# Performance work log

Hardware: AMD Instinct MI355X
Metric: run time of the kernel (lower is better)

## Reference

```python
import jax, jax.numpy as jnp
import numpy as np

USER_SIZE = 100000
ITEM_SIZE = 100000
EMBED = 64
BATCH = 16384


def _xavier(key, fan_in, fan_out):
    # xavier_uniform for a torch Linear(fan_in, fan_out); stored as [in, out]
    limit = float(np.sqrt(6.0 / (fan_in + fan_out)))
    return jax.random.uniform(key, (fan_in, fan_out), jnp.float32, -limit, limit)


def setup_inputs() -> dict:
    key = jax.random.key(0)
    ks = jax.random.split(key, 12)
    inp = {
        "user": jax.random.randint(ks[0], (BATCH,), 0, USER_SIZE),
        "item": jax.random.randint(ks[1], (BATCH,), 0, ITEM_SIZE),
        # embedding tables = Linear(vocab, embed) weights, stored [vocab, embed]
        "W_user_gmf": _xavier(ks[2], USER_SIZE, EMBED),
        "b_user_gmf": jnp.zeros((EMBED,), jnp.float32),
        "W_user_mlp": _xavier(ks[3], USER_SIZE, EMBED),
        "b_user_mlp": jnp.zeros((EMBED,), jnp.float32),
        "W_item_gmf": _xavier(ks[4], ITEM_SIZE, EMBED),
        "b_item_gmf": jnp.zeros((EMBED,), jnp.float32),
        "W_item_mlp": _xavier(ks[5], ITEM_SIZE, EMBED),
        "b_item_mlp": jnp.zeros((EMBED,), jnp.float32),
        # MLP tower (eval mode -> dropout is identity)
        "W1": _xavier(ks[6], 2 * EMBED, 2 * EMBED),
        "b1": jnp.zeros((2 * EMBED,), jnp.float32),
        "W2": _xavier(ks[7], 2 * EMBED, EMBED),
        "b2": jnp.zeros((EMBED,), jnp.float32),
        "W3": _xavier(ks[8], EMBED, EMBED // 2),
        "b3": jnp.zeros((EMBED // 2,), jnp.float32),
        "Wp": _xavier(ks[9], EMBED * 3 // 2, 1),
        "bp": jnp.zeros((1,), jnp.float32),
    }
    return inp


def reference(user, item, W_user_gmf, b_user_gmf, W_user_mlp, b_user_mlp,
              W_item_gmf, b_item_gmf, W_item_mlp, b_item_mlp,
              W1, b1, W2, b2, W3, b3, Wp, bp):
    # one-hot @ Linear(vocab, embed) == row gather from the weight table + bias
    eu_gmf = jax.nn.relu(W_user_gmf[user] + b_user_gmf)  # [B, E]
    eu_mlp = jax.nn.relu(W_user_mlp[user] + b_user_mlp)
    ei_gmf = jax.nn.relu(W_item_gmf[item] + b_item_gmf)
    ei_mlp = jax.nn.relu(W_item_mlp[item] + b_item_mlp)

    out_gmf = eu_gmf * ei_gmf                             # [B, E]
    h = jnp.concatenate([eu_mlp, ei_mlp], axis=-1)        # [B, 2E]
    h = jax.nn.relu(h @ W1 + b1)                          # [B, 2E]
    h = jax.nn.relu(h @ W2 + b2)                          # [B, E]
    h = jax.nn.relu(h @ W3 + b3)                          # [B, E/2]

    concat = jnp.concatenate([out_gmf, h], axis=-1)       # [B, 3E/2]
    pred = jax.nn.sigmoid(concat @ Wp + bp)               # [B, 1]
    return pred.reshape(-1)
```

## Files before the change

kernel.cpp:

```cpp
#include <hip/hip_runtime.h>
#include <math.h>

typedef __attribute__((ext_vector_type(8))) short bf16x8;
typedef __attribute__((ext_vector_type(4))) float f32x4;

#define TPB  256
#define NBLK 256

#define W1T_OFF 0
#define W2T_OFF 34816
#define W3T_OFF 52224
#define SCR_OFF 56832
#define SCR_PW  4352
#define SM_BYTES (SCR_OFF + 4*SCR_PW)

__device__ __forceinline__ unsigned short f2bf(float a){
  unsigned ua = __float_as_uint(a);
  return (unsigned short)((ua + 0x7FFFu + ((ua>>16)&1u)) >> 16);
}
__device__ __forceinline__ unsigned int f2bf_pk(float a, float b){
  return (unsigned int)f2bf(a) | ((unsigned int)f2bf(b) << 16);
}
__device__ __forceinline__ bf16x8 mk_frag(float4 a, float4 ba, float4 b, float4 bb){
  union { bf16x8 v; unsigned int u[4]; } o;
  o.u[0] = f2bf_pk(fmaxf(a.x+ba.x,0.f), fmaxf(a.y+ba.y,0.f));
  o.u[1] = f2bf_pk(fmaxf(a.z+ba.z,0.f), fmaxf(a.w+ba.w,0.f));
  o.u[2] = f2bf_pk(fmaxf(b.x+bb.x,0.f), fmaxf(b.y+bb.y,0.f));
  o.u[3] = f2bf_pk(fmaxf(b.z+bb.z,0.f), fmaxf(b.w+bb.w,0.f));
  return o.v;
}

__launch_bounds__(TPB, 2)
__global__ void ncf_mfma(
    const int* __restrict__ user, const int* __restrict__ item,
    const float* __restrict__ Wug, const float* __restrict__ bug,
    const float* __restrict__ Wum, const float* __restrict__ bum,
    const float* __restrict__ Wig, const float* __restrict__ big,
    const float* __restrict__ Wim, const float* __restrict__ bim,
    const float* __restrict__ W1, const float* __restrict__ b1,
    const float* __restrict__ W2, const float* __restrict__ b2,
    const float* __restrict__ W3, const float* __restrict__ b3,
    const float* __restrict__ Wp, const float* __restrict__ bp,
    float* __restrict__ out)
{
  extern __shared__ __align__(16) char sm[];
  const int t    = threadIdx.x;
  const int lane = t & 63;
  const int w    = t >> 6;
  const int r    = lane & 15;
  const int g    = lane >> 4;
  const int gb   = blockIdx.x * 64 + w * 16 + r;

  const int u  = user[gb];
  const int it = item[gb];
  const float* up = Wum + (size_t)u  * 64;
  const float* ip = Wim + (size_t)it * 64;
  float4 mu0 = *(const float4*)(up + 8*g);
  float4 mu1 = *(const float4*)(up + 8*g + 4);
  float4 mu2 = *(const float4*)(up + 32 + 8*g);
  float4 mu3 = *(const float4*)(up + 32 + 8*g + 4);
  float4 mi0 = *(const float4*)(ip + 8*g);
  float4 mi1 = *(const float4*)(ip + 8*g + 4);
  float4 mi2 = *(const float4*)(ip + 32 + 8*g);
  float4 mi3 = *(const float4*)(ip + 32 + 8*g + 4);
  float4 bu0 = *(const float4*)(bum + 8*g);
  float4 bu1 = *(const float4*)(bum + 8*g + 4);
  float4 bu2 = *(const float4*)(bum + 32 + 8*g);
  float4 bu3 = *(const float4*)(bum + 32 + 8*g + 4);
  float4 bi0 = *(const float4*)(bim + 8*g);
  float4 bi1 = *(const float4*)(bim + 8*g + 4);
  float4 bi2 = *(const float4*)(bim + 32 + 8*g);
  float4 bi3 = *(const float4*)(bim + 32 + 8*g + 4);

  const float* ugp = Wug + (size_t)u  * 64 + 16*g;
  const float* igp = Wig + (size_t)it * 64 + 16*g;
  float4 ga[4], gi[4], gba[4], gbb[4], wpv[4];
  #pragma unroll
  for (int c = 0; c < 4; ++c) {
    ga[c]  = *(const float4*)(ugp + 4*c);
    gi[c]  = *(const float4*)(igp + 4*c);
    gba[c] = *(const float4*)(bug + 16*g + 4*c);
    gbb[c] = *(const float4*)(big + 16*g + 4*c);
    wpv[c] = *(const float4*)(Wp  + 16*g + 4*c);
  }
  float b1v[8], b2v[4], b3v[2], wp3[2];
  #pragma unroll
  for (int i = 0; i < 8; ++i) b1v[i] = b1[i*16 + r];
  #pragma unroll
  for (int i = 0; i < 4; ++i) b2v[i] = b2[i*16 + r];
  #pragma unroll
  for (int i = 0; i < 2; ++i) { b3v[i] = b3[i*16 + r]; wp3[i] = Wp[64 + i*16 + r]; }
  const float bpv = bp[0];

  #pragma unroll
  for (int i = 0; i < 32; ++i) {
    int p = i*TPB + t; int n = p & 127, kp = p >> 7;
    float f0 = W1[(2*kp)*128 + n], f1 = W1[(2*kp+1)*128 + n];
    *(unsigned int*)(sm + W1T_OFF + n*272 + kp*4) = f2bf_pk(f0, f1);
  }
  #pragma unroll
  for (int i = 0; i < 16; ++i) {
    int p = i*TPB + t; int n = p & 63, kp = p >> 6;
    float f0 = W2[(2*kp)*64 + n], f1 = W2[(2*kp+1)*64 + n];
    *(unsigned int*)(sm + W2T_OFF + n*272 + kp*4) = f2bf_pk(f0, f1);
  }
  #pragma unroll
  for (int i = 0; i < 4; ++i) {
    int p = i*TPB + t; int n = p & 31, kp = p >> 5;
    float f0 = W3[(2*kp)*32 + n], f1 = W3[(2*kp+1)*32 + n];
    *(unsigned int*)(sm + W3T_OFF + n*144 + kp*4) = f2bf_pk(f0, f1);
  }

  float psum = 0.f;
  #pragma unroll
  for (int c = 0; c < 4; ++c) {
    psum += fmaxf(ga[c].x+gba[c].x,0.f) * fmaxf(gi[c].x+gbb[c].x,0.f) * wpv[c].x;
    psum += fmaxf(ga[c].y+gba[c].y,0.f) * fmaxf(gi[c].y+gbb[c].y,0.f) * wpv[c].y;
    psum += fmaxf(ga[c].z+gba[c].z,0.f) * fmaxf(gi[c].z+gbb[c].z,0.f) * wpv[c].z;
    psum += fmaxf(ga[c].w+gba[c].w,0.f) * fmaxf(gi[c].w+gbb[c].w,0.f) * wpv[c].w;
  }

  bf16x8 afr[4];
  afr[0] = mk_frag(mu0, bu0, mu1, bu1);
  afr[1] = mk_frag(mu2, bu2, mu3, bu3);
  afr[2] = mk_frag(mi0, bi0, mi1, bi1);
  afr[3] = mk_frag(mi2, bi2, mi3, bi3);

  __syncthreads();

  char* scr = sm + SCR_OFF + w * SCR_PW;

  #pragma unroll
  for (int nt = 0; nt < 8; ++nt) {
    f32x4 acc = {b1v[nt], b1v[nt], b1v[nt], b1v[nt]};
    #pragma unroll
    for (int s = 0; s < 4; ++s) {
      bf16x8 bf = *(const bf16x8*)(sm + W1T_OFF + (nt*16 + r)*272 + s*64 + g*16);
      acc = __builtin_amdgcn_mfma_f32_16x16x32_bf16(afr[s], bf, acc, 0, 0, 0);
    }
    #pragma unroll
    for (int q = 0; q < 4; ++q)
      *(unsigned short*)(scr + (4*g + q)*272 + (nt*16 + r)*2) = f2bf(fmaxf(acc[q], 0.f));
  }

  bf16x8 a2[4];
  #pragma unroll
  for (int s = 0; s < 4; ++s)
    a2[s] = *(const bf16x8*)(scr + r*272 + s*64 + g*16);
  #pragma unroll
  for (int nt = 0; nt < 4; ++nt) {
    f32x4 acc = {b2v[nt], b2v[nt], b2v[nt], b2v[nt]};
    #pragma unroll
    for (int s = 0; s < 4; ++s) {
      bf16x8 bf = *(const bf16x8*)(sm + W2T_OFF + (nt*16 + r)*272 + s*64 + g*16);
      acc = __builtin_amdgcn_mfma_f32_16x16x32_bf16(a2[s], bf, acc, 0, 0, 0);
    }
    #pragma unroll
    for (int q = 0; q < 4; ++q)
      *(unsigned short*)(scr + (4*g + q)*144 + (nt*16 + r)*2) = f2bf(fmaxf(acc[q], 0.f));
  }

  bf16x8 a3[2];
  #pragma unroll
  for (int s = 0; s < 2; ++s)
    a3[s] = *(const bf16x8*)(scr + r*144 + s*64 + g*16);
  float h3p[4] = {0.f, 0.f, 0.f, 0.f};
  #pragma unroll
  for (int nt = 0; nt < 2; ++nt) {
    f32x4 acc = {b3v[nt], b3v[nt], b3v[nt], b3v[nt]};
    #pragma unroll
    for (int s = 0; s < 2; ++s) {
      bf16x8 bf = *(const bf16x8*)(sm + W3T_OFF + (nt*16 + r)*144 + s*64 + g*16);
      acc = __builtin_amdgcn_mfma_f32_16x16x32_bf16(a3[s], bf, acc, 0, 0, 0);
    }
    #pragma unroll
    for (int q = 0; q < 4; ++q)
      h3p[q] += fmaxf(acc[q], 0.f) * wp3[nt];
  }

  float* scf = (float*)scr;
  #pragma unroll
  for (int q = 0; q < 4; ++q) scf[(4*g + q)*20 + r] = h3p[q];
  scf[r*20 + 16 + g] = psum;
  __builtin_amdgcn_wave_barrier();

  if (lane < 16) {
    float x = bpv;
    const float4* row = (const float4*)(scf + lane*20);
    #pragma unroll
    for (int i = 0; i < 5; ++i) { float4 v = row[i]; x += v.x + v.y + v.z + v.w; }
    out[blockIdx.x*64 + w*16 + lane] = 1.f / (1.f + expf(-x));
  }
}

extern "C" void kernel_launch(void* const* d_in, const int* in_sizes, int n_in,
                              void* d_out, int out_size, void* d_ws, size_t ws_size,
                              hipStream_t stream) {
  const int*   user = (const int*)  d_in[0];
  const int*   item = (const int*)  d_in[1];
  const float* Wug  = (const float*)d_in[2];
  const float* bug  = (const float*)d_in[3];
  const float* Wum  = (const float*)d_in[4];
  const float* bum  = (const float*)d_in[5];
  const float* Wig  = (const float*)d_in[6];
  const float* big  = (const float*)d_in[7];
  const float* Wim  = (const float*)d_in[8];
  const float* bim  = (const float*)d_in[9];
  const float* W1   = (const float*)d_in[10];
  const float* b1   = (const float*)d_in[11];
  const float* W2   = (const float*)d_in[12];
  const float* b2   = (const float*)d_in[13];
  const float* W3   = (const float*)d_in[14];
  const float* b3   = (const float*)d_in[15];
  const float* Wp   = (const float*)d_in[16];
  const float* bp   = (const float*)d_in[17];
  float* out = (float*)d_out;

  (void)hipFuncSetAttribute(reinterpret_cast<const void*>(ncf_mfma),
                            hipFuncAttributeMaxDynamicSharedMemorySize, SM_BYTES);
  ncf_mfma<<<NBLK, TPB, SM_BYTES, stream>>>(
      user, item, Wug, bug, Wum, bum, Wig, big, Wim, bim,
      W1, b1, W2, b2, W3, b3, Wp, bp, out);
}
```

Measured before the change: 12.63 us.

## Split GMF and MLP work across separate waves in 512-thread blocks

```diff
diff --git a/kernel.cpp b/kernel.cpp
--- a/kernel.cpp
+++ b/kernel.cpp
@@ -4,7 +4,7 @@
 typedef __attribute__((ext_vector_type(8))) short bf16x8;
 typedef __attribute__((ext_vector_type(4))) float f32x4;
 
-#define TPB  256
+#define TPB  512
 #define NBLK 256
 
 #define W1T_OFF 0
@@ -12,7 +12,8 @@
 #define W3T_OFF 52224
 #define SCR_OFF 56832
 #define SCR_PW  4352
-#define SM_BYTES (SCR_OFF + 4*SCR_PW)
+#define PG_OFF  74240
+#define SM_BYTES (PG_OFF + 1024)
 
 __device__ __forceinline__ unsigned short f2bf(float a){
   unsigned ua = __float_as_uint(a);
@@ -49,147 +50,156 @@
   const int w    = t >> 6;
   const int r    = lane & 15;
   const int g    = lane >> 4;
-  const int gb   = blockIdx.x * 64 + w * 16 + r;
-
-  const int u  = user[gb];
-  const int it = item[gb];
-  const float* up = Wum + (size_t)u  * 64;
-  const float* ip = Wim + (size_t)it * 64;
-  float4 mu0 = *(const float4*)(up + 8*g);
-  float4 mu1 = *(const float4*)(up + 8*g + 4);
-  float4 mu2 = *(const float4*)(up + 32 + 8*g);
-  float4 mu3 = *(const float4*)(up + 32 + 8*g + 4);
-  float4 mi0 = *(const float4*)(ip + 8*g);
-  float4 mi1 = *(const float4*)(ip + 8*g + 4);
-  float4 mi2 = *(const float4*)(ip + 32 + 8*g);
-  float4 mi3 = *(const float4*)(ip + 32 + 8*g + 4);
-  float4 bu0 = *(const float4*)(bum + 8*g);
-  float4 bu1 = *(const float4*)(bum + 8*g + 4);
-  float4 bu2 = *(const float4*)(bum + 32 + 8*g);
-  float4 bu3 = *(const float4*)(bum + 32 + 8*g + 4);
-  float4 bi0 = *(const float4*)(bim + 8*g);
-  float4 bi1 = *(const float4*)(bim + 8*g + 4);
-  float4 bi2 = *(const float4*)(bim + 32 + 8*g);
-  float4 bi3 = *(const float4*)(bim + 32 + 8*g + 4);
-
-  const float* ugp = Wug + (size_t)u  * 64 + 16*g;
-  const float* igp = Wig + (size_t)it * 64 + 16*g;
+  const bool twv = (w < 4);
+  const int  tw  = twv ? w : (w - 4);
+  const int  gb  = blockIdx.x * 64 + tw * 16 + r;
+
+  float4 mu0, mu1, mu2, mu3, mi0, mi1, mi2, mi3;
+  float4 bu0, bu1, bu2, bu3, bi0, bi1, bi2, bi3;
+  float  b1v[8], b2v[4], b3v[2], wp3[2], bpv = 0.f;
   float4 ga[4], gi[4], gba[4], gbb[4], wpv[4];
+
+  if (twv) {
+    const int u  = user[gb];
+    const int it = item[gb];
+    const float* up = Wum + (size_t)u  * 64;
+    const float* ip = Wim + (size_t)it * 64;
+    mu0 = *(const float4*)(up + 8*g);       mu1 = *(const float4*)(up + 8*g + 4);
+    mu2 = *(const float4*)(up + 32 + 8*g);  mu3 = *(const float4*)(up + 32 + 8*g + 4);
+    mi0 = *(const float4*)(ip + 8*g);       mi1 = *(const float4*)(ip + 8*g + 4);
+    mi2 = *(const float4*)(ip + 32 + 8*g);  mi3 = *(const float4*)(ip + 32 + 8*g + 4);
+    bu0 = *(const float4*)(bum + 8*g);      bu1 = *(const float4*)(bum + 8*g + 4);
+    bu2 = *(const float4*)(bum + 32 + 8*g); bu3 = *(const float4*)(bum + 32 + 8*g + 4);
+    bi0 = *(const float4*)(bim + 8*g);      bi1 = *(const float4*)(bim + 8*g + 4);
+    bi2 = *(const float4*)(bim + 32 + 8*g); bi3 = *(const float4*)(bim + 32 + 8*g + 4);
+    #pragma unroll
+    for (int i = 0; i < 8; ++i) b1v[i] = b1[i*16 + r];
+    #pragma unroll
+    for (int i = 0; i < 4; ++i) b2v[i] = b2[i*16 + r];
+    #pragma unroll
+    for (int i = 0; i < 2; ++i) { b3v[i] = b3[i*16 + r]; wp3[i] = Wp[64 + i*16 + r]; }
+    bpv = bp[0];
+  } else {
+    const int u  = user[gb];
+    const int it = item[gb];
+    const float* ugp = Wug + (size_t)u  * 64 + 16*g;
+    const float* igp = Wig + (size_t)it * 64 + 16*g;
+    #pragma unroll
+    for (int c = 0; c < 4; ++c) {
+      ga[c]  = *(const float4*)(ugp + 4*c);
+      gi[c]  = *(const float4*)(igp + 4*c);
+      gba[c] = *(const float4*)(bug + 16*g + 4*c);
+      gbb[c] = *(const float4*)(big + 16*g + 4*c);
+      wpv[c] = *(const float4*)(Wp  + 16*g + 4*c);
+    }
+  }
+
   #pragma unroll
-  for (int c = 0; c < 4; ++c) {
-    ga[c]  = *(const float4*)(ugp + 4*c);
-    gi[c]  = *(const float4*)(igp + 4*c);
-    gba[c] = *(const float4*)(bug + 16*g + 4*c);
-    gbb[c] = *(const float4*)(big + 16*g + 4*c);
-    wpv[c] = *(const float4*)(Wp  + 16*g + 4*c);
-  }
-  float b1v[8], b2v[4], b3v[2], wp3[2];
-  #pragma unroll
-  for (int i = 0; i < 8; ++i) b1v[i] = b1[i*16 + r];
-  #pragma unroll
-  for (int i = 0; i < 4; ++i) b2v[i] = b2[i*16 + r];
-  #pragma unroll
-  for (int i = 0; i < 2; ++i) { b3v[i] = b3[i*16 + r]; wp3[i] = Wp[64 + i*16 + r]; }
-  const float bpv = bp[0];
-
-  #pragma unroll
-  for (int i = 0; i < 32; ++i) {
+  for (int i = 0; i < 16; ++i) {
     int p = i*TPB + t; int n = p & 127, kp = p >> 7;
     float f0 = W1[(2*kp)*128 + n], f1 = W1[(2*kp+1)*128 + n];
     *(unsigned int*)(sm + W1T_OFF + n*272 + kp*4) = f2bf_pk(f0, f1);
   }
   #pragma unroll
-  for (int i = 0; i < 16; ++i) {
+  for (int i = 0; i < 8; ++i) {
     int p = i*TPB + t; int n = p & 63, kp = p >> 6;
     float f0 = W2[(2*kp)*64 + n], f1 = W2[(2*kp+1)*64 + n];
     *(unsigned int*)(sm + W2T_OFF + n*272 + kp*4) = f2bf_pk(f0, f1);
   }
   #pragma unroll
-  for (int i = 0; i < 4; ++i) {
+  for (int i = 0; i < 2; ++i) {
     int p = i*TPB + t; int n = p & 31, kp = p >> 5;
     float f0 = W3[(2*kp)*32 + n], f1 = W3[(2*kp+1)*32 + n];
     *(unsigned int*)(sm + W3T_OFF + n*144 + kp*4) = f2bf_pk(f0, f1);
   }
 
-  float psum = 0.f;
-  #pragma unroll
-  for (int c = 0; c < 4; ++c) {
-    psum += fmaxf(ga[c].x+gba[c].x,0.f) * fmaxf(gi[c].x+gbb[c].x,0.f) * wpv[c].x;
-    psum += fmaxf(ga[c].y+gba[c].y,0.f) * fmaxf(gi[c].y+gbb[c].y,0.f) * wpv[c].y;
-    psum += fmaxf(ga[c].z+gba[c].z,0.f) * fmaxf(gi[c].z+gbb[c].z,0.f) * wpv[c].z;
-    psum += fmaxf(ga[c].w+gba[c].w,0.f) * fmaxf(gi[c].w+gbb[c].w,0.f) * wpv[c].w;
-  }
-
   bf16x8 afr[4];
-  afr[0] = mk_frag(mu0, bu0, mu1, bu1);
-  afr[1] = mk_frag(mu2, bu2, mu3, bu3);
-  afr[2] = mk_frag(mi0, bi0, mi1, bi1);
-  afr[3] = mk_frag(mi2, bi2, mi3, bi3);
+  if (twv) {
+    afr[0] = mk_frag(mu0, bu0, mu1, bu1);
+    afr[1] = mk_frag(mu2, bu2, mu3, bu3);
+    afr[2] = mk_frag(mi0, bi0, mi1, bi1);
+    afr[3] = mk_frag(mi2, bi2, mi3, bi3);
+  } else {
+    float psum = 0.f;
+    #pragma unroll
+    for (int c = 0; c < 4; ++c) {
+      psum += fmaxf(ga[c].x+gba[c].x,0.f) * fmaxf(gi[c].x+gbb[c].x,0.f) * wpv[c].x;
+      psum += fmaxf(ga[c].y+gba[c].y,0.f) * fmaxf(gi[c].y+gbb[c].y,0.f) * wpv[c].y;
+      psum += fmaxf(ga[c].z+gba[c].z,0.f) * fmaxf(gi[c].z+gbb[c].z,0.f) * wpv[c].z;
+      psum += fmaxf(ga[c].w+gba[c].w,0.f) * fmaxf(gi[c].w+gbb[c].w,0.f) * wpv[c].w;
+    }
+    ((float*)(sm + PG_OFF))[tw*64 + r*4 + g] = psum;
+  }
 
   __syncthreads();
 
-  char* scr = sm + SCR_OFF + w * SCR_PW;
-
-  #pragma unroll
-  for (int nt = 0; nt < 8; ++nt) {
-    f32x4 acc = {b1v[nt], b1v[nt], b1v[nt], b1v[nt]};
-    #pragma unroll
-    for (int s = 0; s < 4; ++s) {
-      bf16x8 bf = *(const bf16x8*)(sm + W1T_OFF + (nt*16 + r)*272 + s*64 + g*16);
-      acc = __builtin_amdgcn_mfma_f32_16x16x32_bf16(afr[s], bf, acc, 0, 0, 0);
-    }
-    #pragma unroll
-    for (int q = 0; q < 4; ++q)
-      *(unsigned short*)(scr + (4*g + q)*272 + (nt*16 + r)*2) = f2bf(fmaxf(acc[q], 0.f));
-  }
-
-  bf16x8 a2[4];
-  #pragma unroll
-  for (int s = 0; s < 4; ++s)
-    a2[s] = *(const bf16x8*)(scr + r*272 + s*64 + g*16);
-  #pragma unroll
-  for (int nt = 0; nt < 4; ++nt) {
-    f32x4 acc = {b2v[nt], b2v[nt], b2v[nt], b2v[nt]};
-    #pragma unroll
-    for (int s = 0; s < 4; ++s) {
-      bf16x8 bf = *(const bf16x8*)(sm + W2T_OFF + (nt*16 + r)*272 + s*64 + g*16);
-      acc = __builtin_amdgcn_mfma_f32_16x16x32_bf16(a2[s], bf, acc, 0, 0, 0);
-    }
-    #pragma unroll
-    for (int q = 0; q < 4; ++q)
-      *(unsigned short*)(scr + (4*g + q)*144 + (nt*16 + r)*2) = f2bf(fmaxf(acc[q], 0.f));
-  }
-
-  bf16x8 a3[2];
-  #pragma unroll
-  for (int s = 0; s < 2; ++s)
-    a3[s] = *(const bf16x8*)(scr + r*144 + s*64 + g*16);
-  float h3p[4] = {0.f, 0.f, 0.f, 0.f};
-  #pragma unroll
-  for (int nt = 0; nt < 2; ++nt) {
-    f32x4 acc = {b3v[nt], b3v[nt], b3v[nt], b3v[nt]};
-    #pragma unroll
-    for (int s = 0; s < 2; ++s) {
-      bf16x8 bf = *(const bf16x8*)(sm + W3T_OFF + (nt*16 + r)*144 + s*64 + g*16);
-      acc = __builtin_amdgcn_mfma_f32_16x16x32_bf16(a3[s], bf, acc, 0, 0, 0);
-    }
-    #pragma unroll
-    for (int q = 0; q < 4; ++q)
-      h3p[q] += fmaxf(acc[q], 0.f) * wp3[nt];
-  }
-
-  float* scf = (float*)scr;
-  #pragma unroll
-  for (int q = 0; q < 4; ++q) scf[(4*g + q)*20 + r] = h3p[q];
-  scf[r*20 + 16 + g] = psum;
-  __builtin_amdgcn_wave_barrier();
-
-  if (lane < 16) {
+  if (twv) {
+    char* scr = sm + SCR_OFF + tw * SCR_PW;
+
+    #pragma unroll
+    for (int nt = 0; nt < 8; ++nt) {
+      f32x4 acc = {b1v[nt], b1v[nt], b1v[nt], b1v[nt]};
+      #pragma unroll
+      for (int s = 0; s < 4; ++s) {
+        bf16x8 bf = *(const bf16x8*)(sm + W1T_OFF + (nt*16 + r)*272 + s*64 + g*16);
+        acc = __builtin_amdgcn_mfma_f32_16x16x32_bf16(afr[s], bf, acc, 0, 0, 0);
+      }
+      #pragma unroll
+      for (int q = 0; q < 4; ++q)
+        *(unsigned short*)(scr + (4*g + q)*272 + (nt*16 + r)*2) = f2bf(fmaxf(acc[q], 0.f));
+    }
+
+    bf16x8 a2[4];
+    #pragma unroll
+    for (int s = 0; s < 4; ++s)
+      a2[s] = *(const bf16x8*)(scr + r*272 + s*64 + g*16);
+    #pragma unroll
+    for (int nt = 0; nt < 4; ++nt) {
+      f32x4 acc = {b2v[nt], b2v[nt], b2v[nt], b2v[nt]};
+      #pragma unroll
+      for (int s = 0; s < 4; ++s) {
+        bf16x8 bf = *(const bf16x8*)(sm + W2T_OFF + (nt*16 + r)*272 + s*64 + g*16);
+        acc = __builtin_amdgcn_mfma_f32_16x16x32_bf16(a2[s], bf, acc, 0, 0, 0);
+      }
+      #pragma unroll
+      for (int q = 0; q < 4; ++q)
+        *(unsigned short*)(scr + (4*g + q)*144 + (nt*16 + r)*2) = f2bf(fmaxf(acc[q], 0.f));
+    }
+
+    bf16x8 a3[2];
+    #pragma unroll
+    for (int s = 0; s < 2; ++s)
+      a3[s] = *(const bf16x8*)(scr + r*144 + s*64 + g*16);
+    float h3p[4] = {0.f, 0.f, 0.f, 0.f};
+    #pragma unroll
+    for (int nt = 0; nt < 2; ++nt) {
+      f32x4 acc = {b3v[nt], b3v[nt], b3v[nt], b3v[nt]};
+      #pragma unroll
+      for (int s = 0; s < 2; ++s) {
+        bf16x8 bf = *(const bf16x8*)(sm + W3T_OFF + (nt*16 + r)*144 + s*64 + g*16);
+        acc = __builtin_amdgcn_mfma_f32_16x16x32_bf16(a3[s], bf, acc, 0, 0, 0);
+      }
+      #pragma unroll
+      for (int q = 0; q < 4; ++q)
+        h3p[q] += fmaxf(acc[q], 0.f) * wp3[nt];
+    }
+
+    float* scf = (float*)scr;
+    #pragma unroll
+    for (int q = 0; q < 4; ++q) scf[(4*g + q)*20 + r] = h3p[q];
+  }
+
+  __syncthreads();
+
+  if (twv && lane < 16) {
+    const float* scf = (const float*)(sm + SCR_OFF + tw * SCR_PW);
+    const float4* row = (const float4*)(scf + lane*20);
+    const float4* pg  = (const float4*)((const float*)(sm + PG_OFF) + tw*64 + lane*4);
     float x = bpv;
-    const float4* row = (const float4*)(scf + lane*20);
-    #pragma unroll
-    for (int i = 0; i < 5; ++i) { float4 v = row[i]; x += v.x + v.y + v.z + v.w; }
-    out[blockIdx.x*64 + w*16 + lane] = 1.f / (1.f + expf(-x));
+    #pragma unroll
+    for (int i = 0; i < 4; ++i) { float4 v = row[i]; x += v.x + v.y + v.z + v.w; }
+    { float4 v = pg[0]; x += v.x + v.y + v.z + v.w; }
+    out[blockIdx.x*64 + tw*16 + lane] = 1.f / (1.f + expf(-x));
   }
 }
 
```

After: 12.71 us. About the same (+0.6%).

## Pre-convert MLP weights to bf16 transposed layout in a separate kernel

Applied to the files above, without the earlier changes.

```diff
diff --git a/kernel.cpp b/kernel.cpp
--- a/kernel.cpp
+++ b/kernel.cpp
@@ -3,16 +3,21 @@
 
 typedef __attribute__((ext_vector_type(8))) short bf16x8;
 typedef __attribute__((ext_vector_type(4))) float f32x4;
+typedef __attribute__((ext_vector_type(4))) unsigned int u32x4;
 
 #define TPB  256
 #define NBLK 256
+
+#define WS_W1 0
+#define WS_W2 8192
+#define WS_W3 12288
 
 #define W1T_OFF 0
 #define W2T_OFF 34816
 #define W3T_OFF 52224
 #define SCR_OFF 56832
 #define SCR_PW  4352
-#define SM_BYTES (SCR_OFF + 4*SCR_PW)
+#define SM_BYTES 74240
 
 __device__ __forceinline__ unsigned short f2bf(float a){
   unsigned ua = __float_as_uint(a);
@@ -30,6 +35,21 @@
   return o.v;
 }
 
+__global__ void __launch_bounds__(256) ncf_convert(
+    const float* __restrict__ W1, const float* __restrict__ W2,
+    const float* __restrict__ W3, unsigned int* __restrict__ ws)
+{
+  const int p = blockIdx.x * 256 + threadIdx.x;
+  float f0, f1; int dst;
+  if (p < 8192)       { int kp = p >> 7,            n = p & 127;
+    f0 = W1[(2*kp)*128 + n]; f1 = W1[(2*kp+1)*128 + n]; dst = WS_W1 + n*64 + kp; }
+  else if (p < 12288) { int q = p - 8192,  kp = q >> 6, n = q & 63;
+    f0 = W2[(2*kp)*64  + n]; f1 = W2[(2*kp+1)*64  + n]; dst = WS_W2 + n*64 + kp; }
+  else                { int q = p - 12288, kp = q >> 5, n = q & 31;
+    f0 = W3[(2*kp)*32  + n]; f1 = W3[(2*kp+1)*32  + n]; dst = WS_W3 + n*32 + kp; }
+  ws[dst] = f2bf_pk(f0, f1);
+}
+
 __launch_bounds__(TPB, 2)
 __global__ void ncf_mfma(
     const int* __restrict__ user, const int* __restrict__ item,
@@ -37,10 +57,10 @@
     const float* __restrict__ Wum, const float* __restrict__ bum,
     const float* __restrict__ Wig, const float* __restrict__ big,
     const float* __restrict__ Wim, const float* __restrict__ bim,
-    const float* __restrict__ W1, const float* __restrict__ b1,
-    const float* __restrict__ W2, const float* __restrict__ b2,
-    const float* __restrict__ W3, const float* __restrict__ b3,
+    const float* __restrict__ b1, const float* __restrict__ b2,
+    const float* __restrict__ b3,
     const float* __restrict__ Wp, const float* __restrict__ bp,
+    const unsigned int* __restrict__ ws,
     float* __restrict__ out)
 {
   extern __shared__ __align__(16) char sm[];
@@ -63,69 +83,59 @@
   float4 mi1 = *(const float4*)(ip + 8*g + 4);
   float4 mi2 = *(const float4*)(ip + 32 + 8*g);
   float4 mi3 = *(const float4*)(ip + 32 + 8*g + 4);
-  float4 bu0 = *(const float4*)(bum + 8*g);
-  float4 bu1 = *(const float4*)(bum + 8*g + 4);
-  float4 bu2 = *(const float4*)(bum + 32 + 8*g);
-  float4 bu3 = *(const float4*)(bum + 32 + 8*g + 4);
-  float4 bi0 = *(const float4*)(bim + 8*g);
-  float4 bi1 = *(const float4*)(bim + 8*g + 4);
-  float4 bi2 = *(const float4*)(bim + 32 + 8*g);
-  float4 bi3 = *(const float4*)(bim + 32 + 8*g + 4);
 
   const float* ugp = Wug + (size_t)u  * 64 + 16*g;
   const float* igp = Wig + (size_t)it * 64 + 16*g;
-  float4 ga[4], gi[4], gba[4], gbb[4], wpv[4];
+
+  const u32x4* wsv = (const u32x4*)ws;
+  #pragma unroll
+  for (int i = 0; i < 8; ++i) {
+    int c = i*TPB + t; int n = c >> 4, sub = c & 15;
+    *(u32x4*)(sm + W1T_OFF + n*272 + sub*16) = wsv[c];
+  }
+  #pragma unroll
+  for (int i = 0; i < 4; ++i) {
+    int c = i*TPB + t; int n = c >> 4, sub = c & 15;
+    *(u32x4*)(sm + W2T_OFF + n*272 + sub*16) = wsv[2048 + c];
+  }
+  {
+    int c = t; int n = c >> 3, sub = c & 7;
+    *(u32x4*)(sm + W3T_OFF + n*144 + sub*16) = wsv[3072 + c];
+  }
+
+  float psum = 0.f;
   #pragma unroll
   for (int c = 0; c < 4; ++c) {
-    ga[c]  = *(const float4*)(ugp + 4*c);
-    gi[c]  = *(const float4*)(igp + 4*c);
-    gba[c] = *(const float4*)(bug + 16*g + 4*c);
-    gbb[c] = *(const float4*)(big + 16*g + 4*c);
-    wpv[c] = *(const float4*)(Wp  + 16*g + 4*c);
-  }
-  float b1v[8], b2v[4], b3v[2], wp3[2];
-  #pragma unroll
-  for (int i = 0; i < 8; ++i) b1v[i] = b1[i*16 + r];
-  #pragma unroll
-  for (int i = 0; i < 4; ++i) b2v[i] = b2[i*16 + r];
-  #pragma unroll
-  for (int i = 0; i < 2; ++i) { b3v[i] = b3[i*16 + r]; wp3[i] = Wp[64 + i*16 + r]; }
-  const float bpv = bp[0];
-
-  #pragma unroll
-  for (int i = 0; i < 32; ++i) {
-    int p = i*TPB + t; int n = p & 127, kp = p >> 7;
-    float f0 = W1[(2*kp)*128 + n], f1 = W1[(2*kp+1)*128 + n];
-    *(unsigned int*)(sm + W1T_OFF + n*272 + kp*4) = f2bf_pk(f0, f1);
-  }
-  #pragma unroll
-  for (int i = 0; i < 16; ++i) {
-    int p = i*TPB + t; int n = p & 63, kp = p >> 6;
-    float f0 = W2[(2*kp)*64 + n], f1 = W2[(2*kp+1)*64 + n];
-    *(unsigned int*)(sm + W2T_OFF + n*272 + kp*4) = f2bf_pk(f0, f1);
-  }
-  #pragma unroll
-  for (int i = 0; i < 4; ++i) {
-    int p = i*TPB + t; int n = p & 31, kp = p >> 5;
-    float f0 = W3[(2*kp)*32 + n], f1 = W3[(2*kp+1)*32 + n];
-    *(unsigned int*)(sm + W3T_OFF + n*144 + kp*4) = f2bf_pk(f0, f1);
-  }
-
-  float psum = 0.f;
-  #pragma unroll
-  for (int c = 0; c < 4; ++c) {
-    psum += fmaxf(ga[c].x+gba[c].x,0.f) * fmaxf(gi[c].x+gbb[c].x,0.f) * wpv[c].x;
-    psum += fmaxf(ga[c].y+gba[c].y,0.f) * fmaxf(gi[c].y+gbb[c].y,0.f) * wpv[c].y;
-    psum += fmaxf(ga[c].z+gba[c].z,0.f) * fmaxf(gi[c].z+gbb[c].z,0.f) * wpv[c].z;
-    psum += fmaxf(ga[c].w+gba[c].w,0.f) * fmaxf(gi[c].w+gbb[c].w,0.f) * wpv[c].w;
-  }
-
+    float4 ga  = *(const float4*)(ugp + 4*c);
+    float4 gi  = *(const float4*)(igp + 4*c);
+    float4 gba = *(const float4*)(bug + 16*g + 4*c);
+    float4 gbb = *(const float4*)(big + 16*g + 4*c);
+    float4 wpv = *(const float4*)(Wp  + 16*g + 4*c);
+    psum += fmaxf(ga.x+gba.x,0.f) * fmaxf(gi.x+gbb.x,0.f) * wpv.x;
+    psum += fmaxf(ga.y+gba.y,0.f) * fmaxf(gi.y+gbb.y,0.f) * wpv.y;
+    psum += fmaxf(ga.z+gba.z,0.f) * fmaxf(gi.z+gbb.z,0.f) * wpv.z;
+    psum += fmaxf(ga.w+gba.w,0.f) * fmaxf(gi.w+gbb.w,0.f) * wpv.w;
+  }
+
+  float4 bu0 = *(const float4*)(bum + 8*g);      float4 bu1 = *(const float4*)(bum + 8*g + 4);
+  float4 bu2 = *(const float4*)(bum + 32 + 8*g); float4 bu3 = *(const float4*)(bum + 32 + 8*g + 4);
+  float4 bi0 = *(const float4*)(bim + 8*g);      float4 bi1 = *(const float4*)(bim + 8*g + 4);
+  float4 bi2 = *(const float4*)(bim + 32 + 8*g); float4 bi3 = *(const float4*)(bim + 32 + 8*g + 4);
   bf16x8 afr[4];
   afr[0] = mk_frag(mu0, bu0, mu1, bu1);
   afr[1] = mk_frag(mu2, bu2, mu3, bu3);
   afr[2] = mk_frag(mi0, bi0, mi1, bi1);
   afr[3] = mk_frag(mi2, bi2, mi3, bi3);
 
+  float b1v[8], b2v[4], b3v[2], wp3[2];
+  #pragma unroll
+  for (int i = 0; i < 8; ++i) b1v[i] = b1[i*16 + r];
+  #pragma unroll
+  for (int i = 0; i < 4; ++i) b2v[i] = b2[i*16 + r];
+  #pragma unroll
+  for (int i = 0; i < 2; ++i) { b3v[i] = b3[i*16 + r]; wp3[i] = Wp[64 + i*16 + r]; }
+  const float bpv = bp[0];
+
   __syncthreads();
 
   char* scr = sm + SCR_OFF + w * SCR_PW;
@@ -185,8 +195,8 @@
   __builtin_amdgcn_wave_barrier();
 
   if (lane < 16) {
+    const float4* row = (const float4*)(scf + lane*20);
     float x = bpv;
-    const float4* row = (const float4*)(scf + lane*20);
     #pragma unroll
     for (int i = 0; i < 5; ++i) { float4 v = row[i]; x += v.x + v.y + v.z + v.w; }
     out[blockIdx.x*64 + w*16 + lane] = 1.f / (1.f + expf(-x));
@@ -215,10 +225,13 @@
   const float* Wp   = (const float*)d_in[16];
   const float* bp   = (const float*)d_in[17];
   float* out = (float*)d_out;
+  unsigned int* ws = (unsigned int*)d_ws;
+
+  ncf_convert<<<52, 256, 0, stream>>>(W1, W2, W3, ws);
 
   (void)hipFuncSetAttribute(reinterpret_cast<const void*>(ncf_mfma),
                             hipFuncAttributeMaxDynamicSharedMemorySize, SM_BYTES);
   ncf_mfma<<<NBLK, TPB, SM_BYTES, stream>>>(
       user, item, Wug, bug, Wum, bum, Wig, big, Wim, bim,
-      W1, b1, W2, b2, W3, b3, Wp, bp, out);
-}
+      b1, b2, b3, Wp, bp, ws, out);
+}
```

After: 19.65 us. +55.5%, slower.
